# Kernel optimization log

Measured on AMD Instinct MI355X. Metric: run time of the kernel, lower is better.

## Reference

```python
import jax, jax.numpy as jnp
import numpy as np

N_NODES = 100_000
N_EDGES = 1_200_000
N_GRAPHS = 256
HIT_IN, VAR_IN = 5, 19
H = 64            # hit_embed_dim (h_feat of ResGCN)
D = 128           # transformer hidden = hit + var embed
N_GNN, N_ENC, HEADS, NCLS = 6, 6, 8, 2
EPS = 1e-7        # GENConv message eps


def _ln(x, g, b, eps=1e-5):
    m = jnp.mean(x, -1, keepdims=True)
    v = jnp.mean((x - m) ** 2, -1, keepdims=True)
    return (x - m) * jax.lax.rsqrt(v + eps) * g + b


def _forward(floats, edge_index, batch):
    (x, var_data, enc_W, enc_b, ln_g, ln_b, t_param, mlp1_W, mlp1_b,
     mlpn_g, mlpn_b, mlp2_W, mlp2_b, v1_W, v1_b, v2_W, v2_b, v3_W, v3_b,
     qkv_W, qkv_b, out_W, out_b, ln1_g, ln1_b, ff1_W, ff1_b, ff2_W, ff2_b,
     ln2_g, ln2_b, head_W, head_b) = floats
    src, dst = edge_index[0], edge_index[1]
    N = x.shape[0]
    h = x @ enc_W + enc_b                                   # [N, H]
    for i in range(N_GNN):
        # DeepGCNLayer block='res+': norm -> relu -> conv, then residual add
        z = jax.nn.relu(_ln(h, ln_g[i], ln_b[i]))
        # GENConv aggr='softmax': per-channel segment softmax over incoming edges
        msg = jax.nn.relu(z[src]) + EPS                     # [E, H]
        s = msg * t_param[i]
        m = jax.lax.stop_gradient(jax.ops.segment_max(s, dst, num_segments=N))
        m = jnp.where(jnp.isfinite(m), m, 0.0)
        e = jnp.exp(s - m[dst])
        den = jax.ops.segment_sum(e, dst, num_segments=N)
        alpha = e / jnp.maximum(den, 1e-16)[dst]
        agg = jax.ops.segment_sum(msg * alpha, dst, num_segments=N)
        # GENConv: out = mlp(agg + x_dst); MLP = Lin(H,2H)->LN->ReLU->Lin(2H,H)
        u = z + agg
        u = jax.nn.relu(_ln(u @ mlp1_W[i] + mlp1_b[i], mlpn_g[i], mlpn_b[i]))
        u = u @ mlp2_W[i] + mlp2_b[i]
        h = h + u
    pooled = jax.ops.segment_sum(h, batch, num_segments=N_GRAPHS)  # [B, H]
    # VariableEmbed MLP 19->16->32->64
    v = jax.nn.relu(var_data @ v1_W + v1_b)
    v = jax.nn.relu(v @ v2_W + v2_b)
    v = v @ v3_W + v3_b
    # reshape(-1,1,D) -> seq_len = num_graphs, batch = 1 (post-norm encoder)
    t = jnp.concatenate([pooled, v], -1)                    # [B, D]
    S = t.shape[0]
    dh = D // HEADS
    for i in range(N_ENC):
        qkv = t @ qkv_W[i] + qkv_b[i]
        q, k, vv = jnp.split(qkv, 3, axis=-1)
        q = q.reshape(S, HEADS, dh).transpose(1, 0, 2)
        k = k.reshape(S, HEADS, dh).transpose(1, 0, 2)
        vv = vv.reshape(S, HEADS, dh).transpose(1, 0, 2)
        att = jax.nn.softmax(jnp.einsum('hqd,hkd->hqk', q, k) / jnp.sqrt(jnp.float32(dh)), axis=-1)
        o = jnp.einsum('hqk,hkd->hqd', att, vv).transpose(1, 0, 2).reshape(S, D)
        o = o @ out_W[i] + out_b[i]
        t = _ln(t + o, ln1_g[i], ln1_b[i])
        f = jax.nn.gelu(t @ ff1_W[i] + ff1_b[i], approximate=False)
        f = f @ ff2_W[i] + ff2_b[i]
        t = _ln(t + f, ln2_g[i], ln2_b[i])
    return t @ head_W + head_b                              # [B, NCLS]


FLOAT_KEYS = ['x', 'var_data', 'enc_W', 'enc_b', 'ln_g', 'ln_b', 't_param',
              'mlp1_W', 'mlp1_b', 'mlpn_g', 'mlpn_b', 'mlp2_W', 'mlp2_b',
              'v1_W', 'v1_b', 'v2_W', 'v2_b', 'v3_W', 'v3_b',
              'qkv_W', 'qkv_b', 'out_W', 'out_b', 'ln1_g', 'ln1_b',
              'ff1_W', 'ff1_b', 'ff2_W', 'ff2_b', 'ln2_g', 'ln2_b',
              'head_W', 'head_b']


def setup_inputs() -> dict:
    key = jax.random.key(0)
    ks = iter(jax.random.split(key, 64))
    def nrm(shape, s=0.05):
        return jax.random.normal(next(ks), shape, jnp.float32) * s
    return {
        'x': jax.random.normal(next(ks), (N_NODES, HIT_IN), jnp.float32),
        'edge_index': jax.random.randint(next(ks), (2, N_EDGES), 0, N_NODES),
        'batch': jnp.sort(jax.random.randint(next(ks), (N_NODES,), 0, N_GRAPHS)),
        'var_data': jax.random.normal(next(ks), (N_GRAPHS, VAR_IN), jnp.float32),
        'enc_W': nrm((HIT_IN, H)), 'enc_b': jnp.zeros((H,)),
        'ln_g': jnp.ones((N_GNN, H)), 'ln_b': jnp.zeros((N_GNN, H)),
        't_param': jnp.ones((N_GNN,)),
        'mlp1_W': nrm((N_GNN, H, 2 * H)), 'mlp1_b': jnp.zeros((N_GNN, 2 * H)),
        'mlpn_g': jnp.ones((N_GNN, 2 * H)), 'mlpn_b': jnp.zeros((N_GNN, 2 * H)),
        'mlp2_W': nrm((N_GNN, 2 * H, H)), 'mlp2_b': jnp.zeros((N_GNN, H)),
        'v1_W': nrm((VAR_IN, 16)), 'v1_b': jnp.zeros((16,)),
        'v2_W': nrm((16, 32)), 'v2_b': jnp.zeros((32,)),
        'v3_W': nrm((32, 64)), 'v3_b': jnp.zeros((64,)),
        'qkv_W': nrm((N_ENC, D, 3 * D)), 'qkv_b': jnp.zeros((N_ENC, 3 * D)),
        'out_W': nrm((N_ENC, D, D)), 'out_b': jnp.zeros((N_ENC, D)),
        'ln1_g': jnp.ones((N_ENC, D)), 'ln1_b': jnp.zeros((N_ENC, D)),
        'ff1_W': nrm((N_ENC, D, D)), 'ff1_b': jnp.zeros((N_ENC, D)),
        'ff2_W': nrm((N_ENC, D, D)), 'ff2_b': jnp.zeros((N_ENC, D)),
        'ln2_g': jnp.ones((N_ENC, D)), 'ln2_b': jnp.zeros((N_ENC, D)),
        'head_W': nrm((D, NCLS)), 'head_b': jnp.zeros((NCLS,)),
    }


def reference(x, edge_index, batch, var_data, enc_W, enc_b, ln_g, ln_b, t_param,
              mlp1_W, mlp1_b, mlpn_g, mlpn_b, mlp2_W, mlp2_b,
              v1_W, v1_b, v2_W, v2_b, v3_W, v3_b,
              qkv_W, qkv_b, out_W, out_b, ln1_g, ln1_b,
              ff1_W, ff1_b, ff2_W, ff2_b, ln2_g, ln2_b, head_W, head_b):
    floats = (x, var_data, enc_W, enc_b, ln_g, ln_b, t_param, mlp1_W, mlp1_b,
              mlpn_g, mlpn_b, mlp2_W, mlp2_b, v1_W, v1_b, v2_W, v2_b, v3_W, v3_b,
              qkv_W, qkv_b, out_W, out_b, ln1_g, ln1_b, ff1_W, ff1_b, ff2_W, ff2_b,
              ln2_g, ln2_b, head_W, head_b)
    return _forward(floats, edge_index, batch)
```

## Files before the change

kernel.cpp:

```cpp
#include <hip/hip_runtime.h>
#include <hip/hip_bf16.h>
#include <math.h>

#define NODES 100000
#define EDGES 1200000
#define NG 256

typedef unsigned short u16;
typedef unsigned int   u32;
typedef __attribute__((ext_vector_type(8))) short bf16x8;
typedef __attribute__((ext_vector_type(4))) float f32x4;

__device__ __forceinline__ u16 f2bf(float f){
  u32 u = __float_as_uint(f);
  u32 r = (u + 0x7FFFu + ((u >> 16) & 1u)) >> 16;
  return (u16)r;
}
__device__ __forceinline__ float bf2f(u16 b){ return __uint_as_float(((u32)b) << 16); }

__device__ __forceinline__ float wsum64(float v){
  v += __shfl_xor(v, 32); v += __shfl_xor(v, 16); v += __shfl_xor(v, 8);
  v += __shfl_xor(v, 4);  v += __shfl_xor(v, 2);  v += __shfl_xor(v, 1);
  return v;
}
__device__ __forceinline__ float wmax64(float v){
  v = fmaxf(v, __shfl_xor(v, 32)); v = fmaxf(v, __shfl_xor(v, 16));
  v = fmaxf(v, __shfl_xor(v, 8));  v = fmaxf(v, __shfl_xor(v, 4));
  v = fmaxf(v, __shfl_xor(v, 2));  v = fmaxf(v, __shfl_xor(v, 1));
  return v;
}
__device__ __forceinline__ float bsum256(float v, float* red){
  v = wsum64(v);
  if ((threadIdx.x & 63) == 0) red[threadIdx.x >> 6] = v;
  __syncthreads();
  float r = red[0] + red[1] + red[2] + red[3];
  __syncthreads();
  return r;
}

__global__ void k_zero2(int* counts, float* pooled){
  int i = blockIdx.x*256 + threadIdx.x;
  if (i < NODES) counts[i] = 0;
  if (i < NG*64) pooled[i] = 0.f;
}

__global__ void k_wprep(const float* __restrict__ m1W, const float* __restrict__ m2W,
                        u16* __restrict__ w1t_g, u16* __restrict__ w2t_g){
  int idx = blockIdx.x*256 + threadIdx.x;
  if (idx < 49152){
    int L = idx >> 13, r = idx & 8191, j = r >> 6, k = r & 63;
    w1t_g[idx] = f2bf(m1W[(L << 13) + k*128 + j]);
  } else if (idx < 98304){
    int t = idx - 49152;
    int L = t >> 13, r = t & 8191, j = r >> 7, k = r & 127;
    w2t_g[t] = f2bf(m2W[(L << 13) + k*64 + j]);
  }
}

__global__ void k_hist(const int* __restrict__ dst, int* __restrict__ counts){
  int e = blockIdx.x*256 + threadIdx.x;
  if (e < EDGES) atomicAdd(&counts[dst[e]], 1);
}

__global__ void k_scan1(const int* __restrict__ counts, int* __restrict__ rowptr, int* __restrict__ bsums){
  __shared__ int sd[256];
  int tid = threadIdx.x;
  int base = blockIdx.x*2048 + tid*8;
  int v[8]; int s = 0;
  #pragma unroll
  for (int i = 0; i < 8; i++){
    int idx = base + i;
    int c = (idx < NODES) ? counts[idx] : 0;
    v[i] = s; s += c;
  }
  sd[tid] = s;
  __syncthreads();
  for (int off = 1; off < 256; off <<= 1){
    int t = 0;
    if (tid >= off) t = sd[tid - off];
    __syncthreads();
    if (tid >= off) sd[tid] += t;
    __syncthreads();
  }
  int excl = (tid > 0) ? sd[tid-1] : 0;
  #pragma unroll
  for (int i = 0; i < 8; i++){
    int idx = base + i;
    if (idx < NODES) rowptr[idx] = v[i] + excl;
  }
  if (tid == 255) bsums[blockIdx.x] = sd[255];
}

__global__ void k_scan2(const int* __restrict__ bsums, int* __restrict__ boffs, int nb){
  int tid = threadIdx.x;
  int acc = 0;
  for (int j = 0; j < nb; j++){
    int b = bsums[j];
    if (j < tid) acc += b;
  }
  if (tid < nb) boffs[tid] = acc;
}

__global__ void k_scan3(int* __restrict__ rowptr, int* __restrict__ cursor, const int* __restrict__ boffs){
  int i = blockIdx.x*256 + threadIdx.x;
  if (i < NODES){
    int r = rowptr[i] + boffs[i >> 11];
    rowptr[i] = r; cursor[i] = r;
  }
  if (i == 0) rowptr[NODES] = EDGES;
}

__global__ void k_scatter(const int* __restrict__ src, const int* __restrict__ dst,
                          int* __restrict__ cursor, int* __restrict__ esrc){
  int e = blockIdx.x*256 + threadIdx.x;
  if (e < EDGES){
    int d = dst[e];
    int p = atomicAdd(&cursor[d], 1);
    esrc[p] = src[e];
  }
}

__global__ __launch_bounds__(256) void k_enc(const float* __restrict__ x,
    const float* __restrict__ encW, const float* __restrict__ encb,
    const float* __restrict__ lg, const float* __restrict__ lb,
    float* __restrict__ h, u16* __restrict__ z){
  __shared__ float we[320], wb[64], sg[64], sb[64];
  int tid = threadIdx.x;
  for (int i = tid; i < 320; i += 256) we[i] = encW[i];
  if (tid < 64){ wb[tid] = encb[tid]; sg[tid] = lg[tid]; sb[tid] = lb[tid]; }
  __syncthreads();
  int n = blockIdx.x*256 + tid;
  if (n >= NODES) return;
  float xv[5];
  #pragma unroll
  for (int k = 0; k < 5; k++) xv[k] = x[n*5 + k];
  float a[64];
  #pragma unroll
  for (int c = 0; c < 64; c++){
    float t = wb[c];
    #pragma unroll
    for (int k = 0; k < 5; k++) t += xv[k]*we[k*64 + c];
    a[c] = t;
  }
  float mean = 0.f;
  #pragma unroll
  for (int c = 0; c < 64; c++) mean += a[c];
  mean *= (1.f/64.f);
  float var = 0.f;
  #pragma unroll
  for (int c = 0; c < 64; c++){ float d = a[c]-mean; var += d*d; }
  var *= (1.f/64.f);
  float rstd = rsqrtf(var + 1e-5f);
  size_t rb = (size_t)n*64;
  #pragma unroll
  for (int c = 0; c < 64; c += 4){
    *(float4*)&h[rb + c] = make_float4(a[c], a[c+1], a[c+2], a[c+3]);
    ushort4 zv;
    zv.x = f2bf(fmaxf((a[c  ]-mean)*rstd*sg[c  ]+sb[c  ], 0.f));
    zv.y = f2bf(fmaxf((a[c+1]-mean)*rstd*sg[c+1]+sb[c+1], 0.f));
    zv.z = f2bf(fmaxf((a[c+2]-mean)*rstd*sg[c+2]+sb[c+2], 0.f));
    zv.w = f2bf(fmaxf((a[c+3]-mean)*rstd*sg[c+3]+sb[c+3], 0.f));
    *(ushort4*)&z[rb + c] = zv;
  }
}

__global__ __launch_bounds__(256) void k_agg(const u16* __restrict__ z, u16* __restrict__ u,
    const int* __restrict__ rowptr, const int* __restrict__ esrc,
    const float* __restrict__ tparam, int li){
  int lane = threadIdx.x & 63;
  int n = blockIdx.x*4 + (threadIdx.x >> 6);
  if (n >= NODES) return;
  float tp = tparam[li];
  int beg = rowptr[n], end = rowptr[n+1];
  float zn = bf2f(z[(size_t)n*64 + lane]);
  float den = 0.f, num = 0.f;
  int e = beg;
  for (; e + 7 < end; e += 8){
    int si[8];
    #pragma unroll
    for (int r = 0; r < 8; r++) si[r] = esrc[e + r];
    float mv[8];
    #pragma unroll
    for (int r = 0; r < 8; r++) mv[r] = bf2f(z[(size_t)si[r]*64 + lane]) + 1e-7f;
    #pragma unroll
    for (int r = 0; r < 8; r++){
      float ex = __expf(mv[r]*tp);
      den += ex; num += mv[r]*ex;
    }
  }
  for (; e + 3 < end; e += 4){
    int si[4];
    #pragma unroll
    for (int r = 0; r < 4; r++) si[r] = esrc[e + r];
    float mv[4];
    #pragma unroll
    for (int r = 0; r < 4; r++) mv[r] = bf2f(z[(size_t)si[r]*64 + lane]) + 1e-7f;
    #pragma unroll
    for (int r = 0; r < 4; r++){
      float ex = __expf(mv[r]*tp);
      den += ex; num += mv[r]*ex;
    }
  }
  for (; e < end; ++e){
    int s0 = esrc[e];
    float m0 = bf2f(z[(size_t)s0*64 + lane]) + 1e-7f;
    float e0 = __expf(m0*tp);
    den += e0; num += m0*e0;
  }
  float agg = num / fmaxf(den, 1e-16f);
  u[(size_t)n*64 + lane] = f2bf(zn + agg);
}

__global__ __launch_bounds__(256) void k_mlpm(
    const u16* __restrict__ u, float* __restrict__ h, u16* __restrict__ znext,
    float* __restrict__ pooled, const int* __restrict__ batch,
    const u16* __restrict__ w1t_g, const u16* __restrict__ w2t_g,
    const float* __restrict__ B1, const float* __restrict__ G1, const float* __restrict__ Q1,
    const float* __restrict__ B2, const float* __restrict__ GN, const float* __restrict__ BN,
    int last){
  __shared__ u16 w1t[128*88];
  __shared__ u16 w2t[64*152];
  __shared__ u16 sact[64*152];
  __shared__ float cb1[128], cg1[128], cq1[128];
  __shared__ float cb2[64], cgn[64], cbn[64];
  int tid = threadIdx.x;
  const uint4* w1g = (const uint4*)w1t_g;
  const uint4* w2g = (const uint4*)w2t_g;
  for (int i = tid; i < 1024; i += 256){
    { int j = i >> 3, c = i & 7;  *(uint4*)&w1t[j*88  + c*8] = w1g[i]; }
    { int j = i >> 4, c = i & 15; *(uint4*)&w2t[j*152 + c*8] = w2g[i]; }
  }
  if (tid < 128){ cb1[tid] = B1[tid]; cg1[tid] = G1[tid]; cq1[tid] = Q1[tid]; }
  if (tid < 64){
    cb2[tid] = B2[tid];
    cgn[tid] = last ? 0.f : GN[tid];
    cbn[tid] = last ? 0.f : BN[tid];
  }
  __syncthreads();

  int w = tid >> 6, l = tid & 63, l15 = l & 15, g = l >> 4;
  int nd = w*16 + l15;
  int base0 = blockIdx.x*256;
  f32x4 zero4 = {0.f, 0.f, 0.f, 0.f};
  bf16x8 bz8 = {0,0,0,0,0,0,0,0};

  #pragma unroll 1
  for (int it = 0; it < 4; it++){
    int node = base0 + it*64 + nd;
    bool ok = node < NODES;
    bf16x8 bu0 = ok ? *(const bf16x8*)&u[(size_t)node*64 +      g*8] : bz8;
    bf16x8 bu1 = ok ? *(const bf16x8*)&u[(size_t)node*64 + 32 + g*8] : bz8;
    f32x4 c1[8];
    #pragma unroll
    for (int mt = 0; mt < 8; mt++) c1[mt] = zero4;
    #pragma unroll
    for (int mt = 0; mt < 8; mt++){
      bf16x8 aw0 = *(const bf16x8*)&w1t[(mt*16 + l15)*88 +      g*8];
      c1[mt] = __builtin_amdgcn_mfma_f32_16x16x32_bf16(aw0, bu0, c1[mt], 0, 0, 0);
      bf16x8 aw1 = *(const bf16x8*)&w1t[(mt*16 + l15)*88 + 32 + g*8];
      c1[mt] = __builtin_amdgcn_mfma_f32_16x16x32_bf16(aw1, bu1, c1[mt], 0, 0, 0);
    }
    float sum = 0.f, sq = 0.f;
    #pragma unroll
    for (int mt = 0; mt < 8; mt++){
      #pragma unroll
      for (int r = 0; r < 4; r++){
        float v = c1[mt][r] + cb1[mt*16 + g*4 + r];
        c1[mt][r] = v;
        sum += v; sq += v*v;
      }
    }
    sum += __shfl_xor(sum, 16); sum += __shfl_xor(sum, 32);
    sq  += __shfl_xor(sq, 16);  sq  += __shfl_xor(sq, 32);
    float mean = sum*(1.f/128.f);
    float var  = sq*(1.f/128.f) - mean*mean;
    float rstd = rsqrtf(fmaxf(var, 0.f) + 1e-5f);
    #pragma unroll
    for (int mt = 0; mt < 8; mt++){
      int ch = mt*16 + g*4;
      float a0 = fmaxf((c1[mt][0]-mean)*rstd*cg1[ch  ] + cq1[ch  ], 0.f);
      float a1 = fmaxf((c1[mt][1]-mean)*rstd*cg1[ch+1] + cq1[ch+1], 0.f);
      float a2 = fmaxf((c1[mt][2]-mean)*rstd*cg1[ch+2] + cq1[ch+2], 0.f);
      float a3 = fmaxf((c1[mt][3]-mean)*rstd*cg1[ch+3] + cq1[ch+3], 0.f);
      uint2 pk;
      pk.x = (u32)f2bf(a0) | ((u32)f2bf(a1) << 16);
      pk.y = (u32)f2bf(a2) | ((u32)f2bf(a3) << 16);
      *(uint2*)&sact[nd*152 + ch] = pk;
    }
    f32x4 c2[4];
    #pragma unroll
    for (int mt = 0; mt < 4; mt++) c2[mt] = zero4;
    #pragma unroll
    for (int ks = 0; ks < 4; ks++){
      bf16x8 ba = *(const bf16x8*)&sact[nd*152 + ks*32 + g*8];
      #pragma unroll
      for (int mt = 0; mt < 4; mt++){
        bf16x8 aw = *(const bf16x8*)&w2t[(mt*16 + l15)*152 + ks*32 + g*8];
        c2[mt] = __builtin_amdgcn_mfma_f32_16x16x32_bf16(aw, ba, c2[mt], 0, 0, 0);
      }
    }
    if (ok){
      float out[16];
      size_t hb = (size_t)node*64;
      #pragma unroll
      for (int mt = 0; mt < 4; mt++){
        int ch = mt*16 + g*4;
        float4 hv = *(const float4*)&h[hb + ch];
        out[mt*4  ] = c2[mt][0] + cb2[ch  ] + hv.x;
        out[mt*4+1] = c2[mt][1] + cb2[ch+1] + hv.y;
        out[mt*4+2] = c2[mt][2] + cb2[ch+2] + hv.z;
        out[mt*4+3] = c2[mt][3] + cb2[ch+3] + hv.w;
      }
      if (!last){
        #pragma unroll
        for (int mt = 0; mt < 4; mt++){
          int ch = mt*16 + g*4;
          *(float4*)&h[hb + ch] = make_float4(out[mt*4], out[mt*4+1], out[mt*4+2], out[mt*4+3]);
        }
        float s2 = 0.f, q2 = 0.f;
        #pragma unroll
        for (int c = 0; c < 16; c++){ s2 += out[c]; q2 += out[c]*out[c]; }
        s2 += __shfl_xor(s2, 16); s2 += __shfl_xor(s2, 32);
        q2 += __shfl_xor(q2, 16); q2 += __shfl_xor(q2, 32);
        float m2 = s2*(1.f/64.f);
        float v2 = q2*(1.f/64.f) - m2*m2;
        float rs2 = rsqrtf(fmaxf(v2, 0.f) + 1e-5f);
        #pragma unroll
        for (int mt = 0; mt < 4; mt++){
          int ch = mt*16 + g*4;
          u16 z0 = f2bf(fmaxf((out[mt*4  ]-m2)*rs2*cgn[ch  ] + cbn[ch  ], 0.f));
          u16 z1 = f2bf(fmaxf((out[mt*4+1]-m2)*rs2*cgn[ch+1] + cbn[ch+1], 0.f));
          u16 z2 = f2bf(fmaxf((out[mt*4+2]-m2)*rs2*cgn[ch+2] + cbn[ch+2], 0.f));
          u16 z3 = f2bf(fmaxf((out[mt*4+3]-m2)*rs2*cgn[ch+3] + cbn[ch+3], 0.f));
          uint2 pk; pk.x = (u32)z0 | ((u32)z1 << 16); pk.y = (u32)z2 | ((u32)z3 << 16);
          *(uint2*)&znext[hb + ch] = pk;
        }
      } else {
        int gb = batch[node];
        #pragma unroll
        for (int c = 0; c < 16; c++){
          int ch = (c >> 2)*16 + g*4 + (c & 3);
          atomicAdd(&pooled[gb*64 + ch], out[c]);
        }
      }
    }
  }
}

__global__ __launch_bounds__(128) void k_pool2(
    const float* __restrict__ pooled, const float* __restrict__ var_data,
    const float* __restrict__ v1W, const float* __restrict__ v1b,
    const float* __restrict__ v2W, const float* __restrict__ v2b,
    const float* __restrict__ v3W, const float* __restrict__ v3b,
    float* __restrict__ t, float* __restrict__ qkvout,
    const float* __restrict__ qW, const float* __restrict__ qb){
  __shared__ float vin[19], l1[16], l2[32], tr[128];
  int c = threadIdx.x, s = blockIdx.x;
  if (c < 19) vin[c] = var_data[s*19 + c];
  __syncthreads();
  if (c < 16){
    float a = v1b[c];
    for (int k = 0; k < 19; k++) a += vin[k]*v1W[k*16 + c];
    l1[c] = fmaxf(a, 0.f);
  }
  __syncthreads();
  if (c < 32){
    float a = v2b[c];
    for (int k = 0; k < 16; k++) a += l1[k]*v2W[k*32 + c];
    l2[c] = fmaxf(a, 0.f);
  }
  __syncthreads();
  float tv;
  if (c < 64) tv = pooled[s*64 + c];
  else {
    float a = v3b[c-64];
    for (int k = 0; k < 32; k++) a += l2[k]*v3W[k*64 + (c-64)];
    tv = a;
  }
  tr[c] = tv; t[s*128 + c] = tv;
  __syncthreads();
  #pragma unroll 1
  for (int r = 0; r < 3; r++){
    int col = r*128 + c;
    float a = qb[col];
    #pragma unroll 4
    for (int k = 0; k < 128; k++) a += tr[k]*qW[k*384 + col];
    qkvout[s*384 + col] = a;
  }
}

__global__ __launch_bounds__(256) void k_attrow(
    const float* __restrict__ qkv, float* __restrict__ t, float* __restrict__ qkvout,
    const float* __restrict__ outW, const float* __restrict__ outb,
    const float* __restrict__ l1g, const float* __restrict__ l1b,
    const float* __restrict__ f1W, const float* __restrict__ f1b,
    const float* __restrict__ f2W, const float* __restrict__ f2b,
    const float* __restrict__ l2g, const float* __restrict__ l2b,
    const float* __restrict__ qW, const float* __restrict__ qb,
    const float* __restrict__ hW, const float* __restrict__ hb2,
    float* __restrict__ dout, int last){
  __shared__ float kv[8448];
  __shared__ float sc[8*260];
  __shared__ float qrow[128], orow[128], strow[128], s1row[128], sfrow[128], t2row[128];
  __shared__ float red[4];
  int tid = threadIdx.x, s = blockIdx.x;
  if (tid < 128){ qrow[tid] = qkv[(size_t)s*384 + tid]; strow[tid] = t[(size_t)s*128 + tid]; }
  for (int tile = 0; tile < 4; tile++){
    __syncthreads();
    for (int i = tid; i < 8192; i += 256){
      int r = i >> 7, c = i & 127;
      kv[r*132 + c] = qkv[(size_t)(tile*64 + r)*384 + 128 + c];
    }
    __syncthreads();
    int j = tid >> 2, sub = tid & 3;
    float d0 = 0.f, d1 = 0.f;
    #pragma unroll
    for (int d = 0; d < 16; d++){
      d0 += qrow[sub*16 + d]     * kv[j*132 + sub*16 + d];
      d1 += qrow[(sub+4)*16 + d] * kv[j*132 + (sub+4)*16 + d];
    }
    sc[sub*260     + tile*64 + j] = d0*0.25f;
    sc[(sub+4)*260 + tile*64 + j] = d1*0.25f;
  }
  __syncthreads();
  {
    int wid = tid >> 6, lane = tid & 63;
    #pragma unroll
    for (int hh = 0; hh < 2; hh++){
      int hh2 = wid*2 + hh;
      float a0 = sc[hh2*260 + lane], a1 = sc[hh2*260 + 64 + lane];
      float a2 = sc[hh2*260 + 128 + lane], a3 = sc[hh2*260 + 192 + lane];
      float m = wmax64(fmaxf(fmaxf(a0,a1), fmaxf(a2,a3)));
      float e0 = __expf(a0-m), e1 = __expf(a1-m), e2 = __expf(a2-m), e3 = __expf(a3-m);
      float sum = wsum64((e0+e1)+(e2+e3));
      float inv = 1.f/sum;
      sc[hh2*260 + lane] = e0*inv; sc[hh2*260 + 64 + lane] = e1*inv;
      sc[hh2*260 + 128 + lane] = e2*inv; sc[hh2*260 + 192 + lane] = e3*inv;
    }
  }
  float o = 0.f;
  int hme = (tid & 127) >> 4;
  for (int tile = 0; tile < 4; tile++){
    __syncthreads();
    for (int i = tid; i < 8192; i += 256){
      int r = i >> 7, c = i & 127;
      kv[r*132 + c] = qkv[(size_t)(tile*64 + r)*384 + 256 + c];
    }
    __syncthreads();
    if (tid < 128){
      #pragma unroll 4
      for (int j = 0; j < 64; j++)
        o += sc[hme*260 + tile*64 + j] * kv[j*132 + tid];
    }
  }
  if (tid < 128) orow[tid] = o;
  float acc = (tid < 128) ? outb[tid] : 0.f;
  for (int kt = 0; kt < 4; kt++){
    __syncthreads();
    for (int i = tid; i < 4096; i += 256) kv[i] = outW[(size_t)kt*4096 + i];
    __syncthreads();
    if (tid < 128){
      #pragma unroll 8
      for (int kk = 0; kk < 32; kk++) acc += orow[kt*32 + kk]*kv[kk*128 + tid];
    }
  }
  if (tid < 128) acc += strow[tid];
  float mean = bsum256((tid < 128) ? acc : 0.f, red)*(1.f/128.f);
  float d0v = (tid < 128) ? (acc - mean) : 0.f;
  float var = bsum256(d0v*d0v, red)*(1.f/128.f);
  float t1 = 0.f;
  if (tid < 128){
    t1 = d0v*rsqrtf(var + 1e-5f)*l1g[tid] + l1b[tid];
    s1row[tid] = t1;
  }
  float f = (tid < 128) ? f1b[tid] : 0.f;
  for (int kt = 0; kt < 4; kt++){
    __syncthreads();
    for (int i = tid; i < 4096; i += 256) kv[i] = f1W[(size_t)kt*4096 + i];
    __syncthreads();
    if (tid < 128){
      #pragma unroll 8
      for (int kk = 0; kk < 32; kk++) f += s1row[kt*32 + kk]*kv[kk*128 + tid];
    }
  }
  if (tid < 128){
    f = 0.5f*f*(1.f + erff(f*0.70710678118654752f));
    sfrow[tid] = f;
  }
  float g = (tid < 128) ? f2b[tid] : 0.f;
  for (int kt = 0; kt < 4; kt++){
    __syncthreads();
    for (int i = tid; i < 4096; i += 256) kv[i] = f2W[(size_t)kt*4096 + i];
    __syncthreads();
    if (tid < 128){
      #pragma unroll 8
      for (int kk = 0; kk < 32; kk++) g += sfrow[kt*32 + kk]*kv[kk*128 + tid];
    }
  }
  if (tid < 128) g += t1;
  float mean2 = bsum256((tid < 128) ? g : 0.f, red)*(1.f/128.f);
  float d2v = (tid < 128) ? (g - mean2) : 0.f;
  float var2 = bsum256(d2v*d2v, red)*(1.f/128.f);
  if (tid < 128){
    float t2 = d2v*rsqrtf(var2 + 1e-5f)*l2g[tid] + l2b[tid];
    t[(size_t)s*128 + tid] = t2;
    t2row[tid] = t2;
  }
  __syncthreads();
  if (!last){
    float a0 = qb[tid];
    float a1 = (tid < 128) ? qb[256 + tid] : 0.f;
    for (int kt = 0; kt < 8; kt++){
      __syncthreads();
      for (int i = tid; i < 6144; i += 256) kv[i] = qW[(size_t)kt*6144 + i];
      __syncthreads();
      #pragma unroll 4
      for (int kk = 0; kk < 16; kk++){
        float tv = t2row[kt*16 + kk];
        a0 += tv*kv[kk*384 + tid];
        if (tid < 128) a1 += tv*kv[kk*384 + 256 + tid];
      }
    }
    qkvout[(size_t)s*384 + tid] = a0;
    if (tid < 128) qkvout[(size_t)s*384 + 256 + tid] = a1;
  } else {
    if (tid < 2){
      float a = hb2[tid];
      for (int k = 0; k < 128; k++) a += t2row[k]*hW[k*2 + tid];
      dout[s*2 + tid] = a;
    }
  }
}

extern "C" void kernel_launch(void* const* d_in, const int* in_sizes, int n_in,
                              void* d_out, int out_size, void* d_ws, size_t ws_size,
                              hipStream_t stream){
  const float* x       = (const float*)d_in[0];
  const int*   ei      = (const int*)  d_in[1];
  const int*   batch   = (const int*)  d_in[2];
  const float* var_d   = (const float*)d_in[3];
  const float* encW    = (const float*)d_in[4];
  const float* encb    = (const float*)d_in[5];
  const float* ln_g    = (const float*)d_in[6];
  const float* ln_b    = (const float*)d_in[7];
  const float* tparam  = (const float*)d_in[8];
  const float* m1W     = (const float*)d_in[9];
  const float* m1b     = (const float*)d_in[10];
  const float* mng     = (const float*)d_in[11];
  const float* mnb     = (const float*)d_in[12];
  const float* m2W     = (const float*)d_in[13];
  const float* m2b     = (const float*)d_in[14];
  const float* v1W     = (const float*)d_in[15];
  const float* v1b     = (const float*)d_in[16];
  const float* v2W     = (const float*)d_in[17];
  const float* v2b     = (const float*)d_in[18];
  const float* v3W     = (const float*)d_in[19];
  const float* v3b     = (const float*)d_in[20];
  const float* qkvW    = (const float*)d_in[21];
  const float* qkvB    = (const float*)d_in[22];
  const float* outW    = (const float*)d_in[23];
  const float* outb    = (const float*)d_in[24];
  const float* l1g     = (const float*)d_in[25];
  const float* l1b     = (const float*)d_in[26];
  const float* f1W     = (const float*)d_in[27];
  const float* f1b     = (const float*)d_in[28];
  const float* f2W     = (const float*)d_in[29];
  const float* f2b     = (const float*)d_in[30];
  const float* l2g     = (const float*)d_in[31];
  const float* l2b     = (const float*)d_in[32];
  const float* headW   = (const float*)d_in[33];
  const float* headB   = (const float*)d_in[34];
  float* dout = (float*)d_out;

  char* wsb = (char*)d_ws;
  size_t off = 0;
  auto nxt = [&](size_t bytes)->void*{
    void* p = wsb + off;
    off += (bytes + 255) & ~(size_t)255;
    return p;
  };
  float* h      = (float*)nxt((size_t)NODES*64*4);
  u16*   z      = (u16*)  nxt((size_t)NODES*64*2);
  u16*   u      = (u16*)  nxt((size_t)NODES*64*2);
  int*   rowptr = (int*)  nxt((size_t)(NODES+1)*4);
  int*   cursor = (int*)  nxt((size_t)NODES*4);
  int*   counts = (int*)  nxt((size_t)NODES*4);
  int*   bsums  = (int*)  nxt(64*4);
  int*   boffs  = (int*)  nxt(64*4);
  int*   esrc   = (int*)  nxt((size_t)EDGES*4);
  float* pooled = (float*)nxt((size_t)NG*64*4);
  float* tbuf   = (float*)nxt((size_t)NG*128*4);
  float* qkv0   = (float*)nxt((size_t)NG*384*4);
  float* qkv1   = (float*)nxt((size_t)NG*384*4);
  u16*   w1tg   = (u16*)  nxt((size_t)49152*2);
  u16*   w2tg   = (u16*)  nxt((size_t)49152*2);
  float* qkvb[2] = { qkv0, qkv1 };

  const int* srcp = ei;
  const int* dstp = ei + EDGES;

  k_zero2  <<<391, 256, 0, stream>>>(counts, pooled);
  k_wprep  <<<384, 256, 0, stream>>>(m1W, m2W, w1tg, w2tg);
  k_hist   <<<4688, 256, 0, stream>>>(dstp, counts);
  k_scan1  <<<49, 256, 0, stream>>>(counts, rowptr, bsums);
  k_scan2  <<<1, 64, 0, stream>>>(bsums, boffs, 49);
  k_scan3  <<<391, 256, 0, stream>>>(rowptr, cursor, boffs);
  k_scatter<<<4688, 256, 0, stream>>>(srcp, dstp, cursor, esrc);
  k_enc    <<<391, 256, 0, stream>>>(x, encW, encb, ln_g, ln_b, h, z);

  for (int i = 0; i < 6; i++){
    int last = (i == 5);
    k_agg <<<25000, 256, 0, stream>>>(z, u, rowptr, esrc, tparam, i);
    k_mlpm<<<391, 256, 0, stream>>>(u, h, z, pooled, batch,
        w1tg + i*8192, w2tg + i*8192,
        m1b + i*128, mng + i*128, mnb + i*128,
        m2b + i*64,
        ln_g + (last ? 0 : (i+1)*64), ln_b + (last ? 0 : (i+1)*64), last);
  }

  k_pool2<<<NG, 128, 0, stream>>>(pooled, var_d, v1W, v1b, v2W, v2b, v3W, v3b,
                                  tbuf, qkv0, qkvW, qkvB);

  for (int i = 0; i < 6; i++){
    int last = (i == 5);
    k_attrow<<<NG, 256, 0, stream>>>(qkvb[i & 1], tbuf, qkvb[(i + 1) & 1],
        outW + i*16384, outb + i*128, l1g + i*128, l1b + i*128,
        f1W + i*16384, f1b + i*128, f2W + i*16384, f2b + i*128,
        l2g + i*128, l2b + i*128,
        qkvW + (size_t)(last ? 0 : (i+1))*49152, qkvB + (last ? 0 : (i+1))*384,
        headW, headB, dout, last);
  }
}
```

Before: 1.541 ms.

## Pack bf16 pairs in aggregation and shuffle MLP activations through registers

```diff
diff --git a/kernel.cpp b/kernel.cpp
--- a/kernel.cpp
+++ b/kernel.cpp
@@ -17,6 +17,8 @@
   return (u16)r;
 }
 __device__ __forceinline__ float bf2f(u16 b){ return __uint_as_float(((u32)b) << 16); }
+__device__ __forceinline__ float bfL(u32 v){ return __uint_as_float(v << 16); }
+__device__ __forceinline__ float bfH(u32 v){ return __uint_as_float(v & 0xFFFF0000u); }
 
 __device__ __forceinline__ float wsum64(float v){
   v += __shfl_xor(v, 32); v += __shfl_xor(v, 16); v += __shfl_xor(v, 8);
@@ -164,51 +166,60 @@
   }
 }
 
-__global__ __launch_bounds__(256) void k_agg(const u16* __restrict__ z, u16* __restrict__ u,
+__global__ __launch_bounds__(256) void k_agg(const u32* __restrict__ z32, u32* __restrict__ uo,
     const int* __restrict__ rowptr, const int* __restrict__ esrc,
     const float* __restrict__ tparam, int li){
   int lane = threadIdx.x & 63;
-  int n = blockIdx.x*4 + (threadIdx.x >> 6);
+  int half = lane >> 5;
+  int c2 = lane & 31;
+  int n = blockIdx.x*8 + (threadIdx.x >> 6)*2 + half;
   if (n >= NODES) return;
   float tp = tparam[li];
   int beg = rowptr[n], end = rowptr[n+1];
-  float zn = bf2f(z[(size_t)n*64 + lane]);
-  float den = 0.f, num = 0.f;
+  u32 zp = z32[(size_t)n*32 + c2];
+  float zn0 = bfL(zp), zn1 = bfH(zp);
+  float den0 = 0.f, num0 = 0.f, den1 = 0.f, num1 = 0.f;
   int e = beg;
   for (; e + 7 < end; e += 8){
     int si[8];
     #pragma unroll
     for (int r = 0; r < 8; r++) si[r] = esrc[e + r];
-    float mv[8];
-    #pragma unroll
-    for (int r = 0; r < 8; r++) mv[r] = bf2f(z[(size_t)si[r]*64 + lane]) + 1e-7f;
+    u32 vv[8];
+    #pragma unroll
+    for (int r = 0; r < 8; r++) vv[r] = z32[(size_t)si[r]*32 + c2];
     #pragma unroll
     for (int r = 0; r < 8; r++){
-      float ex = __expf(mv[r]*tp);
-      den += ex; num += mv[r]*ex;
+      float m0 = bfL(vv[r]) + 1e-7f, m1 = bfH(vv[r]) + 1e-7f;
+      float e0 = __expf(m0*tp), e1 = __expf(m1*tp);
+      den0 += e0; num0 += m0*e0;
+      den1 += e1; num1 += m1*e1;
     }
   }
   for (; e + 3 < end; e += 4){
     int si[4];
     #pragma unroll
     for (int r = 0; r < 4; r++) si[r] = esrc[e + r];
-    float mv[4];
-    #pragma unroll
-    for (int r = 0; r < 4; r++) mv[r] = bf2f(z[(size_t)si[r]*64 + lane]) + 1e-7f;
+    u32 vv[4];
+    #pragma unroll
+    for (int r = 0; r < 4; r++) vv[r] = z32[(size_t)si[r]*32 + c2];
     #pragma unroll
     for (int r = 0; r < 4; r++){
-      float ex = __expf(mv[r]*tp);
-      den += ex; num += mv[r]*ex;
+      float m0 = bfL(vv[r]) + 1e-7f, m1 = bfH(vv[r]) + 1e-7f;
+      float e0 = __expf(m0*tp), e1 = __expf(m1*tp);
+      den0 += e0; num0 += m0*e0;
+      den1 += e1; num1 += m1*e1;
     }
   }
   for (; e < end; ++e){
-    int s0 = esrc[e];
-    float m0 = bf2f(z[(size_t)s0*64 + lane]) + 1e-7f;
-    float e0 = __expf(m0*tp);
-    den += e0; num += m0*e0;
-  }
-  float agg = num / fmaxf(den, 1e-16f);
-  u[(size_t)n*64 + lane] = f2bf(zn + agg);
+    u32 v = z32[(size_t)esrc[e]*32 + c2];
+    float m0 = bfL(v) + 1e-7f, m1 = bfH(v) + 1e-7f;
+    float e0 = __expf(m0*tp), e1 = __expf(m1*tp);
+    den0 += e0; num0 += m0*e0;
+    den1 += e1; num1 += m1*e1;
+  }
+  float u0 = zn0 + num0 / fmaxf(den0, 1e-16f);
+  float u1 = zn1 + num1 / fmaxf(den1, 1e-16f);
+  uo[(size_t)n*32 + c2] = (u32)f2bf(u0) | ((u32)f2bf(u1) << 16);
 }
 
 __global__ __launch_bounds__(256) void k_mlpm(
@@ -220,7 +231,6 @@
     int last){
   __shared__ u16 w1t[128*88];
   __shared__ u16 w2t[64*152];
-  __shared__ u16 sact[64*152];
   __shared__ float cb1[128], cg1[128], cq1[128];
   __shared__ float cb2[64], cgn[64], cbn[64];
   int tid = threadIdx.x;
@@ -240,25 +250,35 @@
 
   int w = tid >> 6, l = tid & 63, l15 = l & 15, g = l >> 4;
   int nd = w*16 + l15;
-  int base0 = blockIdx.x*256;
+  int base0 = blockIdx.x*128;
+  int hi = g >> 1;
+  int s0l = ((g & 1) << 5) + l15;
+  int s1l = s0l + 16;
   f32x4 zero4 = {0.f, 0.f, 0.f, 0.f};
   bf16x8 bz8 = {0,0,0,0,0,0,0,0};
 
-  #pragma unroll 1
-  for (int it = 0; it < 4; it++){
+  bf16x8 buA[2], buB[2];
+  #pragma unroll
+  for (int it = 0; it < 2; it++){
     int node = base0 + it*64 + nd;
     bool ok = node < NODES;
-    bf16x8 bu0 = ok ? *(const bf16x8*)&u[(size_t)node*64 +      g*8] : bz8;
-    bf16x8 bu1 = ok ? *(const bf16x8*)&u[(size_t)node*64 + 32 + g*8] : bz8;
+    buA[it] = ok ? *(const bf16x8*)&u[(size_t)node*64 +      g*8] : bz8;
+    buB[it] = ok ? *(const bf16x8*)&u[(size_t)node*64 + 32 + g*8] : bz8;
+  }
+
+  #pragma unroll
+  for (int it = 0; it < 2; it++){
+    int node = base0 + it*64 + nd;
+    bool ok = node < NODES;
     f32x4 c1[8];
     #pragma unroll
     for (int mt = 0; mt < 8; mt++) c1[mt] = zero4;
     #pragma unroll
     for (int mt = 0; mt < 8; mt++){
       bf16x8 aw0 = *(const bf16x8*)&w1t[(mt*16 + l15)*88 +      g*8];
-      c1[mt] = __builtin_amdgcn_mfma_f32_16x16x32_bf16(aw0, bu0, c1[mt], 0, 0, 0);
+      c1[mt] = __builtin_amdgcn_mfma_f32_16x16x32_bf16(aw0, buA[it], c1[mt], 0, 0, 0);
       bf16x8 aw1 = *(const bf16x8*)&w1t[(mt*16 + l15)*88 + 32 + g*8];
-      c1[mt] = __builtin_amdgcn_mfma_f32_16x16x32_bf16(aw1, bu1, c1[mt], 0, 0, 0);
+      c1[mt] = __builtin_amdgcn_mfma_f32_16x16x32_bf16(aw1, buB[it], c1[mt], 0, 0, 0);
     }
     float sum = 0.f, sq = 0.f;
     #pragma unroll
@@ -275,6 +295,7 @@
     float mean = sum*(1.f/128.f);
     float var  = sq*(1.f/128.f) - mean*mean;
     float rstd = rsqrtf(fmaxf(var, 0.f) + 1e-5f);
+    u32 pk0[8], pk1[8];
     #pragma unroll
     for (int mt = 0; mt < 8; mt++){
       int ch = mt*16 + g*4;
@@ -282,21 +303,29 @@
       float a1 = fmaxf((c1[mt][1]-mean)*rstd*cg1[ch+1] + cq1[ch+1], 0.f);
       float a2 = fmaxf((c1[mt][2]-mean)*rstd*cg1[ch+2] + cq1[ch+2], 0.f);
       float a3 = fmaxf((c1[mt][3]-mean)*rstd*cg1[ch+3] + cq1[ch+3], 0.f);
-      uint2 pk;
-      pk.x = (u32)f2bf(a0) | ((u32)f2bf(a1) << 16);
-      pk.y = (u32)f2bf(a2) | ((u32)f2bf(a3) << 16);
-      *(uint2*)&sact[nd*152 + ch] = pk;
+      pk0[mt] = (u32)f2bf(a0) | ((u32)f2bf(a1) << 16);
+      pk1[mt] = (u32)f2bf(a2) | ((u32)f2bf(a3) << 16);
     }
     f32x4 c2[4];
     #pragma unroll
     for (int mt = 0; mt < 4; mt++) c2[mt] = zero4;
     #pragma unroll
     for (int ks = 0; ks < 4; ks++){
-      bf16x8 ba = *(const bf16x8*)&sact[nd*152 + ks*32 + g*8];
+      u32 x0 = pk0[2*ks], x1 = pk0[2*ks+1];
+      u32 y0 = pk1[2*ks], y1 = pk1[2*ks+1];
+      u32 a0 = (u32)__shfl((int)x0, s0l), a1 = (u32)__shfl((int)x1, s0l);
+      u32 b0 = (u32)__shfl((int)y0, s0l), b1 = (u32)__shfl((int)y1, s0l);
+      u32 c0 = (u32)__shfl((int)x0, s1l), c1v = (u32)__shfl((int)x1, s1l);
+      u32 d0 = (u32)__shfl((int)y0, s1l), d1 = (u32)__shfl((int)y1, s1l);
+      union { u32 q[4]; bf16x8 v; } bb;
+      bb.q[0] = hi ? a1 : a0;
+      bb.q[1] = hi ? b1 : b0;
+      bb.q[2] = hi ? c1v : c0;
+      bb.q[3] = hi ? d1 : d0;
       #pragma unroll
       for (int mt = 0; mt < 4; mt++){
         bf16x8 aw = *(const bf16x8*)&w2t[(mt*16 + l15)*152 + ks*32 + g*8];
-        c2[mt] = __builtin_amdgcn_mfma_f32_16x16x32_bf16(aw, ba, c2[mt], 0, 0, 0);
+        c2[mt] = __builtin_amdgcn_mfma_f32_16x16x32_bf16(aw, bb.v, c2[mt], 0, 0, 0);
       }
     }
     if (ok){
@@ -610,8 +639,8 @@
 
   for (int i = 0; i < 6; i++){
     int last = (i == 5);
-    k_agg <<<25000, 256, 0, stream>>>(z, u, rowptr, esrc, tparam, i);
-    k_mlpm<<<391, 256, 0, stream>>>(u, h, z, pooled, batch,
+    k_agg <<<12500, 256, 0, stream>>>((const u32*)z, (u32*)u, rowptr, esrc, tparam, i);
+    k_mlpm<<<782, 256, 0, stream>>>(u, h, z, pooled, batch,
         w1tg + i*8192, w2tg + i*8192,
         m1b + i*128, mng + i*128, mnb + i*128,
         m2b + i*64,
```

After: 1.501 ms. -2.6%, faster.
